# Performance work log

Hardware: AMD Instinct MI355X
Metric: run time of the kernel (lower is better)

Reference implementation:

```python
import jax, jax.numpy as jnp
import numpy as np

D_IN = 512
SEQ_LEN = 4096
CHUNK = 256
NUM_CHUNKS = SEQ_LEN // CHUNK
BATCH = 4


def _xavier_uniform(key, d_in, d_out):
    limit = float(np.sqrt(6.0 / (d_in + d_out)))
    return jax.random.uniform(key, (d_in, d_out), dtype=jnp.float32, minval=-limit, maxval=limit)


def _logit(p, eps=1e-06):
    p = min(max(p, eps), 1.0 - eps)
    return jnp.asarray(np.log(p / (1.0 - p)), dtype=jnp.float32)


def setup_inputs() -> dict:
    key = jax.random.key(0)
    ks = jax.random.split(key, 6)
    x = jax.random.normal(ks[0], (BATCH, SEQ_LEN, D_IN), dtype=jnp.float32)
    return {
        "x": x,
        "w_q": _xavier_uniform(ks[1], D_IN, D_IN),
        "w_k": _xavier_uniform(ks[2], D_IN, D_IN),
        "w_v": _xavier_uniform(ks[3], D_IN, D_IN),
        "mem_w1": _xavier_uniform(ks[4], D_IN, 2 * D_IN),
        "mem_w2": _xavier_uniform(ks[5], 2 * D_IN, D_IN),
        "alpha_t": _logit(0.001),  # unconstrained; sigmoid -> alpha
        "lr_t": _logit(0.01),
        "decay_t": _logit(0.9),
        "update_mem": 1,
    }


def _mem_fwd(h, W1, W2):
    # LinearMLPMemory depth=2: x @ W1 -> gelu -> @ W2 (torch F.gelu is exact erf)
    return jax.nn.gelu(h @ W1, approximate=False) @ W2


def reference(x, w_q, w_k, w_v, mem_w1, mem_w2, alpha_t, lr_t, decay_t, update_mem):
    alpha = jax.nn.sigmoid(alpha_t)
    lr = jax.nn.sigmoid(lr_t)
    decay = jax.nn.sigmoid(decay_t)

    def loss_fn(Ws, k, v):
        W1, W2 = Ws
        pred = _mem_fwd(k, W1, W2)
        return jnp.mean((pred - v) ** 2)

    grad_fn = jax.grad(loss_fn)

    def step(carry, chunk):
        # chunk: [B, CHUNK, D]
        W1, W2, S1, S2 = carry
        k = chunk @ w_k
        v = chunk @ w_v
        g1, g2 = grad_fn((W1, W2), k, v)
        S1 = decay * S1 - lr * g1  # surprise (momentum of negative grads)
        S2 = decay * S2 - lr * g2
        W1 = (1.0 - alpha) * W1 + S1  # weight decay + surprise update
        W2 = (1.0 - alpha) * W2 + S2
        return (W1, W2, S1, S2), None

    W1, W2 = mem_w1, mem_w2
    if update_mem:
        B, S, D = x.shape
        # [NUM_CHUNKS, B, CHUNK, D]: sequential store over chunks (parallelize=False)
        chunks = x.reshape(B, NUM_CHUNKS, CHUNK, D).transpose(1, 0, 2, 3)
        init = (W1, W2, jnp.zeros_like(W1), jnp.zeros_like(W2))
        (W1, W2, _, _), _ = jax.lax.scan(step, init, chunks)

    q = x @ w_q
    return _mem_fwd(q, W1, W2)
```

## Files before the change

### kernel.cpp

```cpp
#include <hip/hip_runtime.h>
#include <math.h>

#define D_IN    512
#define HID     1024
#define CHUNK_L 256
#define NCHUNK  16
#define SEQ_L   4096
#define ROWS    1024
#define NROWS_T 16384

typedef __attribute__((ext_vector_type(4))) float f32x4;
typedef __attribute__((ext_vector_type(8))) short bf16x8;
typedef __attribute__((ext_vector_type(4))) short bf16x4;

#define LOSS_SCALE (2.0f / 524288.0f)

__device__ __forceinline__ float gelu_f(float v) {
    return v * 0.5f * (1.0f + erff(v * 0.70710678118654752f));
}
__device__ __forceinline__ float dgelu_f(float v) {
    float cdf = 0.5f * (1.0f + erff(v * 0.70710678118654752f));
    float pdf = 0.3989422804014327f * expf(-0.5f * v * v);
    return cdf + v * pdf;
}
__device__ __forceinline__ float sigmoid_dev(float x) { return 1.0f / (1.0f + expf(-x)); }
__device__ __forceinline__ short f2b(float f) {
    unsigned u = __float_as_uint(f);
    u += 0x7fffu + ((u >> 16) & 1u);
    return (short)(u >> 16);
}
__device__ __forceinline__ float b2f(short s) {
    return __uint_as_float(((unsigned)(unsigned short)s) << 16);
}
__device__ __forceinline__ float read_scalar(const float* p) {
    float v = *p;
    if (fabsf(v) > 0.5f && fabsf(v) < 16.0f) return v;
    unsigned short lo = ((const unsigned short*)p)[0];
    return __uint_as_float(((unsigned)lo) << 16);
}

__device__ __forceinline__ void glds16(const short* g, short* l) {
    __builtin_amdgcn_global_load_lds(
        (const __attribute__((address_space(1))) void*)g,
        (__attribute__((address_space(3))) void*)l, 16, 0, 0);
}

#define VMWAIT(N) asm volatile("s_waitcnt vmcnt(" #N ")" ::: "memory")

template<int NKB, int NSLOT>
__device__ __forceinline__ void tile_gemm2(
    const short* __restrict__ A, int lda,
    const short* __restrict__ B, int ldb,
    int m0, int n0, short* KB, f32x4 acc[2][2])
{
    const int tid = threadIdx.x;
    const int lane = tid & 63, wave = tid >> 6;
    const int wy = (wave >> 1) * 32, wx = (wave & 1) * 32;
    const int l16 = lane & 15, q = lane >> 4;

    const int ga = tid, gb = tid + 256;
    const int ra = ga >> 3, ja = ga & 7;
    const int rb = gb >> 3, jb = gb & 7;
    const short* sA0 = A + (size_t)(m0 + ra) * lda + ((ja ^ (ra & 7)) << 3);
    const short* sA1 = A + (size_t)(m0 + rb) * lda + ((jb ^ (rb & 7)) << 3);
    const short* sB0 = B + (size_t)(n0 + ra) * ldb + ((ja ^ (ra & 7)) << 3);
    const short* sB1 = B + (size_t)(n0 + rb) * ldb + ((jb ^ (rb & 7)) << 3);

    f32x4 z = {0.f, 0.f, 0.f, 0.f};
    acc[0][0] = z; acc[0][1] = z; acc[1][0] = z; acc[1][1] = z;

    auto issue = [&](int kb) {
        const int ko = kb << 6;
        short* d = KB + (kb % NSLOT) * 8192 + wave * 512;
        glds16(sA0 + ko, d);
        glds16(sA1 + ko, d + 2048);
        glds16(sB0 + ko, d + 4096);
        glds16(sB1 + ko, d + 6144);
    };
#pragma unroll
    for (int kb = 0; kb < NSLOT - 1 && kb < NKB; ++kb) issue(kb);

#pragma unroll
    for (int j = 0; j < NKB; ++j) {
        int ah = NKB - 1 - j; if (ah > NSLOT - 2) ah = NSLOT - 2;
        if      (ah >= 6) VMWAIT(24);
        else if (ah == 5) VMWAIT(20);
        else if (ah == 4) VMWAIT(16);
        else if (ah == 3) VMWAIT(12);
        else if (ah == 2) VMWAIT(8);
        else if (ah == 1) VMWAIT(4);
        else              VMWAIT(0);
        __builtin_amdgcn_s_barrier();
        __builtin_amdgcn_sched_barrier(0);
        if (j + NSLOT - 1 < NKB) issue(j + NSLOT - 1);
        const short* sl = KB + (j % NSLOT) * 8192;
#pragma unroll
        for (int ks = 0; ks < 2; ++ks) {
            bf16x8 af[2], bf[2];
#pragma unroll
            for (int i = 0; i < 2; ++i) {
                int row = wy + i * 16 + l16;
                af[i] = *(const bf16x8*)&sl[(row << 6) + (((ks * 4 + q) ^ (row & 7)) << 3)];
            }
#pragma unroll
            for (int jj = 0; jj < 2; ++jj) {
                int row = wx + jj * 16 + l16;
                bf[jj] = *(const bf16x8*)&sl[4096 + (row << 6) + (((ks * 4 + q) ^ (row & 7)) << 3)];
            }
#pragma unroll
            for (int i = 0; i < 2; ++i)
#pragma unroll
                for (int jj = 0; jj < 2; ++jj)
                    acc[i][jj] = __builtin_amdgcn_mfma_f32_16x16x32_bf16(af[i], bf[jj], acc[i][jj], 0, 0, 0);
        }
    }
}

#define EPI_IDX() \
    const int tid_ = threadIdx.x; \
    const int wy_  = ((tid_ >> 6) >> 1) * 32; \
    const int wxl_ = ((tid_ >> 6) & 1) * 32; \
    const int q4_  = ((tid_ & 63) >> 4) * 4; \
    const int l16_ = tid_ & 15;

__global__ __launch_bounds__(256)
void init_all(const float* __restrict__ w_q, const float* __restrict__ w_k,
              const float* __restrict__ w_v, const float* __restrict__ m1,
              const float* __restrict__ m2,
              float* __restrict__ W1f, float* __restrict__ W2f,
              float* __restrict__ S1, float* __restrict__ S2,
              short* __restrict__ WkvT, short* __restrict__ wqT,
              short* __restrict__ W1bT, short* __restrict__ W2bT,
              short* __restrict__ W2bn)
{
    int i = blockIdx.x * 256 + threadIdx.x;
    float w1 = m1[i], w2 = m2[i];
    W1f[i] = w1; S1[i] = 0.f;
    W2f[i] = w2; S2[i] = 0.f;
    W2bn[i] = f2b(w2);
    int n9 = i >> 9, k9 = i & 511;
    W1bT[i] = f2b(m1[(size_t)k9 * HID + n9]);
    WkvT[i] = f2b(n9 < 512 ? w_k[(size_t)k9 * D_IN + n9]
                           : w_v[(size_t)k9 * D_IN + (n9 - 512)]);
    if (i < 262144) wqT[i] = f2b(w_q[(size_t)k9 * D_IN + n9]);
    int n10 = i >> 10, k10 = i & 1023;
    W2bT[i] = f2b(m2[(size_t)k10 * D_IN + n10]);
}

__global__ __launch_bounds__(256)
void xb_kernel(const float* __restrict__ x, short* __restrict__ xb)
{
    int i = blockIdx.x * 256 + threadIdx.x;
    f32x4 a = ((const f32x4*)x)[i * 2];
    f32x4 b = ((const f32x4*)x)[i * 2 + 1];
    bf16x8 o;
#pragma unroll
    for (int u = 0; u < 4; ++u) { o[u] = f2b(a[u]); o[u + 4] = f2b(b[u]); }
    ((bf16x8*)xb)[i] = o;
}

__global__ __launch_bounds__(256)
void kvq_kernel(const short* __restrict__ xb, const short* __restrict__ WkvT,
                const short* __restrict__ wqT,
                short* __restrict__ KVall, short* __restrict__ Ktall,
                short* __restrict__ qall)
{
    __shared__ short KB[3 * 8192];
    const int bid = blockIdx.x;
    EPI_IDX();
    f32x4 acc[2][2];
    if (bid < 4096) {
        int t = bid >> 8, tile = bid & 255;
        int m0 = (tile & 15) * 64, n0 = (tile >> 4) * 64;
        const short* Akv = xb + ((size_t)(m0 >> 8) * SEQ_L + (size_t)t * CHUNK_L + (m0 & 255)) * D_IN;
        tile_gemm2<8, 3>(Akv, D_IN, WkvT, D_IN, 0, n0, KB, acc);
        short* KV = KVall + (size_t)t * ROWS * 1024;
        short* Kt = Ktall + (size_t)t * D_IN * 1024;
#pragma unroll
        for (int i = 0; i < 2; ++i)
#pragma unroll
            for (int j = 0; j < 2; ++j) {
                int m = m0 + wy_ + i * 16 + q4_, n = n0 + wxl_ + j * 16 + l16_;
                bf16x4 pk;
#pragma unroll
                for (int r = 0; r < 4; ++r) {
                    short b = f2b(acc[i][j][r]);
                    KV[(size_t)(m + r) * 1024 + n] = b;
                    pk[r] = b;
                }
                if (n < 512) *(bf16x4*)&Kt[(size_t)n * 1024 + m] = pk;
            }
    } else {
        int idx = bid - 4096;
        int m0 = (idx & 255) * 64, n0 = (idx >> 8) * 64;
        tile_gemm2<8, 3>(xb, D_IN, wqT, D_IN, m0, n0, KB, acc);
#pragma unroll
        for (int i = 0; i < 2; ++i)
#pragma unroll
            for (int j = 0; j < 2; ++j) {
                int m = m0 + wy_ + i * 16 + q4_, n = n0 + wxl_ + j * 16 + l16_;
#pragma unroll
                for (int r = 0; r < 4; ++r)
                    qall[(size_t)(m + r) * D_IN + n] = f2b(acc[i][j][r]);
            }
    }
}

__global__ __launch_bounds__(256)
void h_kernel(const short* __restrict__ KVt, const short* __restrict__ W1bT,
              short* __restrict__ Gb, short* __restrict__ GbT, short* __restrict__ DG)
{
    __shared__ short KB[8 * 8192];
    const int bid = blockIdx.x;
    EPI_IDX();
    int m0 = (bid & 15) * 64, n0 = (bid >> 4) * 64;
    f32x4 acc[2][2];
    tile_gemm2<8, 8>(KVt, 1024, W1bT, D_IN, m0, n0, KB, acc);
#pragma unroll
    for (int i = 0; i < 2; ++i)
#pragma unroll
        for (int j = 0; j < 2; ++j) {
            int m = m0 + wy_ + i * 16 + q4_, n = n0 + wxl_ + j * 16 + l16_;
            bf16x4 pg;
#pragma unroll
            for (int r = 0; r < 4; ++r) {
                float v = acc[i][j][r];
                float g = gelu_f(v);
                Gb[(size_t)(m + r) * 1024 + n] = f2b(g);
                DG[(size_t)(m + r) * 1024 + n] = f2b(dgelu_f(v));
                pg[r] = f2b(g);
            }
            *(bf16x4*)&GbT[(size_t)n * 1024 + m] = pg;
        }
}

__global__ __launch_bounds__(256)
void e_kernel(const short* __restrict__ Gb, const short* __restrict__ W2bT,
              short* __restrict__ KVt, short* __restrict__ EVt)
{
    __shared__ short KB[8 * 8192];
    const int bid = blockIdx.x;
    EPI_IDX();
    int m0 = (bid & 15) * 64, n0 = (bid >> 4) * 64;
    f32x4 acc[2][2];
    tile_gemm2<16, 8>(Gb, HID, W2bT, HID, m0, n0, KB, acc);
#pragma unroll
    for (int i = 0; i < 2; ++i)
#pragma unroll
        for (int j = 0; j < 2; ++j) {
            int m = m0 + wy_ + i * 16 + q4_, n = n0 + wxl_ + j * 16 + l16_;
            bf16x4 pe;
#pragma unroll
            for (int r = 0; r < 4; ++r) {
                size_t ci = (size_t)(m + r) * 1024 + 512 + n;
                float e = (acc[i][j][r] - b2f(KVt[ci])) * LOSS_SCALE;
                KVt[ci] = f2b(e);
                pe[r] = f2b(e);
            }
            *(bf16x4*)&EVt[(size_t)n * 1024 + m] = pe;
        }
}

__global__ __launch_bounds__(256)
void dh_kernel(const short* __restrict__ KVt, const short* __restrict__ W2bn,
               const short* __restrict__ DG, short* __restrict__ DHt)
{
    __shared__ short KB[8 * 8192];
    const int bid = blockIdx.x;
    EPI_IDX();
    int m0 = (bid & 15) * 64, n0 = (bid >> 4) * 64;
    f32x4 acc[2][2];
    tile_gemm2<8, 8>(KVt + 512, 1024, W2bn, D_IN, m0, n0, KB, acc);
#pragma unroll
    for (int i = 0; i < 2; ++i)
#pragma unroll
        for (int j = 0; j < 2; ++j) {
            int m = m0 + wy_ + i * 16 + q4_, n = n0 + wxl_ + j * 16 + l16_;
            bf16x4 pd;
#pragma unroll
            for (int r = 0; r < 4; ++r)
                pd[r] = f2b(acc[i][j][r] * b2f(DG[(size_t)(m + r) * 1024 + n]));
            *(bf16x4*)&DHt[(size_t)n * 1024 + m] = pd;
        }
}

__global__ __launch_bounds__(256)
void g21_kernel(const short* __restrict__ GbT, const short* __restrict__ EVt,
                const short* __restrict__ Ktt, const short* __restrict__ DHt,
                float* __restrict__ W2f, float* __restrict__ S2,
                short* __restrict__ W2bT, short* __restrict__ W2bn,
                float* __restrict__ W1f, float* __restrict__ S1,
                short* __restrict__ W1bT,
                const float* __restrict__ ap, const float* __restrict__ lp,
                const float* __restrict__ dp, const int* __restrict__ um)
{
    __shared__ short KB[8 * 8192];
    const int bid = blockIdx.x;
    EPI_IDX();
    f32x4 acc[2][2];
    if (bid < 128) {
        int m0 = (bid & 15) * 64, n0 = (bid >> 4) * 64;
        tile_gemm2<16, 8>(GbT, ROWS, EVt, ROWS, m0, n0, KB, acc);
        if (*um != 0) {
            const float alpha = sigmoid_dev(read_scalar(ap));
            const float lr    = sigmoid_dev(read_scalar(lp));
            const float decay = sigmoid_dev(read_scalar(dp));
#pragma unroll
            for (int i = 0; i < 2; ++i)
#pragma unroll
                for (int j = 0; j < 2; ++j) {
                    int m = m0 + wy_ + i * 16 + q4_, n = n0 + wxl_ + j * 16 + l16_;
                    bf16x4 pw;
#pragma unroll
                    for (int r = 0; r < 4; ++r) {
                        size_t ci = (size_t)(m + r) * D_IN + n;
                        float s = decay * S2[ci] - lr * acc[i][j][r];
                        S2[ci] = s;
                        float w = (1.0f - alpha) * W2f[ci] + s;
                        W2f[ci] = w;
                        W2bn[ci] = f2b(w);
                        pw[r] = f2b(w);
                    }
                    *(bf16x4*)&W2bT[(size_t)n * 1024 + m] = pw;
                }
        }
    } else {
        int idx = bid - 128;
        int m0 = (idx & 7) * 64, n0 = (idx >> 3) * 64;
        tile_gemm2<16, 8>(Ktt, ROWS, DHt, ROWS, m0, n0, KB, acc);
        if (*um != 0) {
            const float alpha = sigmoid_dev(read_scalar(ap));
            const float lr    = sigmoid_dev(read_scalar(lp));
            const float decay = sigmoid_dev(read_scalar(dp));
#pragma unroll
            for (int i = 0; i < 2; ++i)
#pragma unroll
                for (int j = 0; j < 2; ++j) {
                    int m = m0 + wy_ + i * 16 + q4_, n = n0 + wxl_ + j * 16 + l16_;
                    bf16x4 pw;
#pragma unroll
                    for (int r = 0; r < 4; ++r) {
                        size_t ci = (size_t)(m + r) * HID + n;
                        float s = decay * S1[ci] - lr * acc[i][j][r];
                        S1[ci] = s;
                        float w = (1.0f - alpha) * W1f[ci] + s;
                        W1f[ci] = w;
                        pw[r] = f2b(w);
                    }
                    *(bf16x4*)&W1bT[(size_t)n * D_IN + m] = pw;
                }
        }
    }
}

__global__ __launch_bounds__(256)
void ro_h_kernel(const short* __restrict__ qall, const short* __restrict__ W1bT,
                 short* __restrict__ Hro)
{
    __shared__ short KB[3 * 8192];
    const int bid = blockIdx.x;
    EPI_IDX();
    int m0 = (bid & 255) * 64, n0 = (bid >> 8) * 64;
    f32x4 acc[2][2];
    tile_gemm2<8, 3>(qall, D_IN, W1bT, D_IN, m0, n0, KB, acc);
#pragma unroll
    for (int i = 0; i < 2; ++i)
#pragma unroll
        for (int j = 0; j < 2; ++j) {
            int m = m0 + wy_ + i * 16 + q4_, n = n0 + wxl_ + j * 16 + l16_;
#pragma unroll
            for (int r = 0; r < 4; ++r)
                Hro[(size_t)(m + r) * HID + n] = f2b(gelu_f(acc[i][j][r]));
        }
}

__global__ __launch_bounds__(256)
void ro_o_kernel(const short* __restrict__ Hro, const short* __restrict__ W2bT,
                 float* __restrict__ out)
{
    __shared__ short KB[3 * 8192];
    const int bid = blockIdx.x;
    EPI_IDX();
    int m0 = (bid & 255) * 64, n0 = (bid >> 8) * 64;
    f32x4 acc[2][2];
    tile_gemm2<16, 3>(Hro, HID, W2bT, HID, m0, n0, KB, acc);
#pragma unroll
    for (int i = 0; i < 2; ++i)
#pragma unroll
        for (int j = 0; j < 2; ++j) {
            int m = m0 + wy_ + i * 16 + q4_, n = n0 + wxl_ + j * 16 + l16_;
#pragma unroll
            for (int r = 0; r < 4; ++r)
                out[(size_t)(m + r) * D_IN + n] = acc[i][j][r];
        }
}

extern "C" void kernel_launch(void* const* d_in, const int* in_sizes, int n_in,
                              void* d_out, int out_size, void* d_ws, size_t ws_size,
                              hipStream_t stream)
{
    const float* x      = (const float*)d_in[0];
    const float* w_q    = (const float*)d_in[1];
    const float* w_k    = (const float*)d_in[2];
    const float* w_v    = (const float*)d_in[3];
    const float* mem_w1 = (const float*)d_in[4];
    const float* mem_w2 = (const float*)d_in[5];
    const float* ap     = (const float*)d_in[6];
    const float* lp     = (const float*)d_in[7];
    const float* dpp    = (const float*)d_in[8];
    const int*   um     = (const int*)d_in[9];
    float* out = (float*)d_out;

    const int nW = D_IN * HID;
    float* W1f = (float*)d_ws;
    float* W2f = W1f + nW;
    float* S1  = W2f + nW;
    float* S2  = S1 + nW;
    short* p   = (short*)(S2 + nW);
    short* WkvT = p;            p += nW;
    short* wqT  = p;            p += 256 * 1024;
    short* W1bT = p;            p += nW;
    short* W2bT = p;            p += nW;
    short* W2bn = p;            p += nW;
    short* Gb   = p;            p += ROWS * HID;
    short* GbT  = p;            p += ROWS * HID;
    short* DG   = p;            p += ROWS * HID;
    short* EVt  = p;            p += ROWS * D_IN;
    short* DHt  = p;            p += ROWS * HID;
    short* qall = p;            p += (size_t)NROWS_T * D_IN;
    short* KVall = p;           p += (size_t)NCHUNK * ROWS * 1024;
    short* Ktall = p;           p += (size_t)NCHUNK * D_IN * 1024;
    short* Hro  = p;            p += (size_t)NROWS_T * HID;
    short* xb   = p;            p += (size_t)NROWS_T * D_IN;

    dim3 blk(256);
    hipLaunchKernelGGL(init_all, dim3(nW / 256), blk, 0, stream,
                       w_q, w_k, w_v, mem_w1, mem_w2,
                       W1f, W2f, S1, S2, WkvT, wqT, W1bT, W2bT, W2bn);
    hipLaunchKernelGGL(xb_kernel, dim3(4096), blk, 0, stream, x, xb);
    hipLaunchKernelGGL(kvq_kernel, dim3(6144), blk, 0, stream,
                       xb, WkvT, wqT, KVall, Ktall, qall);

    for (int t = 0; t < NCHUNK; ++t) {
        short* KVt  = KVall + (size_t)t * ROWS * 1024;
        short* Ktt  = Ktall + (size_t)t * D_IN * 1024;
        hipLaunchKernelGGL(h_kernel, dim3(256), blk, 0, stream, KVt, W1bT, Gb, GbT, DG);
        hipLaunchKernelGGL(e_kernel, dim3(128), blk, 0, stream, Gb, W2bT, KVt, EVt);
        hipLaunchKernelGGL(dh_kernel, dim3(256), blk, 0, stream, KVt, W2bn, DG, DHt);
        hipLaunchKernelGGL(g21_kernel, dim3(256), blk, 0, stream,
                           GbT, EVt, Ktt, DHt, W2f, S2, W2bT, W2bn,
                           W1f, S1, W1bT, ap, lp, dpp, um);
    }

    hipLaunchKernelGGL(ro_h_kernel, dim3(4096), blk, 0, stream, qall, W1bT, Hro);
    hipLaunchKernelGGL(ro_o_kernel, dim3(2048), blk, 0, stream, Hro, W2bT, out);
}
```

Before: 749.4 us.

## Make KVQ and readout blocks loop over N-tiles; fuse readout GEMMs

The KVQ projection now launches one block per 64-row strip that loops over all N-tiles, instead of one block per output tile. The two readout GEMMs are merged into a single kernel: each block computes its 64-row strip of the GELU hidden layer, then reuses it for the second GEMM, with a barrier between the phases. The goal is fewer launches and better cache reuse of each A strip. The cost is far fewer blocks (256 to 512 on a large GPU), which lowers occupancy and parallelism, and the deeper LDS buffers may reduce how many blocks fit per CU.

```diff
diff --git a/kernel.cpp b/kernel.cpp
--- a/kernel.cpp
+++ b/kernel.cpp
@@ -165,44 +165,48 @@
                 short* __restrict__ KVall, short* __restrict__ Ktall,
                 short* __restrict__ qall)
 {
-    __shared__ short KB[3 * 8192];
-    const int bid = blockIdx.x;
-    EPI_IDX();
-    f32x4 acc[2][2];
-    if (bid < 4096) {
-        int t = bid >> 8, tile = bid & 255;
-        int m0 = (tile & 15) * 64, n0 = (tile >> 4) * 64;
+    __shared__ short KB[4 * 8192];
+    const int bid = blockIdx.x;
+    EPI_IDX();
+    f32x4 acc[2][2];
+    if (bid < 256) {
+        int t = bid >> 4, m0 = (bid & 15) * 64;
         const short* Akv = xb + ((size_t)(m0 >> 8) * SEQ_L + (size_t)t * CHUNK_L + (m0 & 255)) * D_IN;
-        tile_gemm2<8, 3>(Akv, D_IN, WkvT, D_IN, 0, n0, KB, acc);
         short* KV = KVall + (size_t)t * ROWS * 1024;
         short* Kt = Ktall + (size_t)t * D_IN * 1024;
-#pragma unroll
-        for (int i = 0; i < 2; ++i)
-#pragma unroll
-            for (int j = 0; j < 2; ++j) {
-                int m = m0 + wy_ + i * 16 + q4_, n = n0 + wxl_ + j * 16 + l16_;
-                bf16x4 pk;
-#pragma unroll
-                for (int r = 0; r < 4; ++r) {
-                    short b = f2b(acc[i][j][r]);
-                    KV[(size_t)(m + r) * 1024 + n] = b;
-                    pk[r] = b;
+        for (int nt = 0; nt < 16; ++nt) {
+            int n0 = nt * 64;
+            tile_gemm2<8, 4>(Akv, D_IN, WkvT, D_IN, 0, n0, KB, acc);
+#pragma unroll
+            for (int i = 0; i < 2; ++i)
+#pragma unroll
+                for (int j = 0; j < 2; ++j) {
+                    int m = m0 + wy_ + i * 16 + q4_, n = n0 + wxl_ + j * 16 + l16_;
+                    bf16x4 pk;
+#pragma unroll
+                    for (int r = 0; r < 4; ++r) {
+                        short b = f2b(acc[i][j][r]);
+                        KV[(size_t)(m + r) * 1024 + n] = b;
+                        pk[r] = b;
+                    }
+                    if (n < 512) *(bf16x4*)&Kt[(size_t)n * 1024 + m] = pk;
                 }
-                if (n < 512) *(bf16x4*)&Kt[(size_t)n * 1024 + m] = pk;
-            }
+        }
     } else {
-        int idx = bid - 4096;
-        int m0 = (idx & 255) * 64, n0 = (idx >> 8) * 64;
-        tile_gemm2<8, 3>(xb, D_IN, wqT, D_IN, m0, n0, KB, acc);
-#pragma unroll
-        for (int i = 0; i < 2; ++i)
-#pragma unroll
-            for (int j = 0; j < 2; ++j) {
-                int m = m0 + wy_ + i * 16 + q4_, n = n0 + wxl_ + j * 16 + l16_;
-#pragma unroll
-                for (int r = 0; r < 4; ++r)
-                    qall[(size_t)(m + r) * D_IN + n] = f2b(acc[i][j][r]);
-            }
+        int m0 = (bid - 256) * 64;
+        for (int nt = 0; nt < 8; ++nt) {
+            int n0 = nt * 64;
+            tile_gemm2<8, 4>(xb, D_IN, wqT, D_IN, m0, n0, KB, acc);
+#pragma unroll
+            for (int i = 0; i < 2; ++i)
+#pragma unroll
+                for (int j = 0; j < 2; ++j) {
+                    int m = m0 + wy_ + i * 16 + q4_, n = n0 + wxl_ + j * 16 + l16_;
+#pragma unroll
+                    for (int r = 0; r < 4; ++r)
+                        qall[(size_t)(m + r) * D_IN + n] = f2b(acc[i][j][r]);
+                }
+        }
     }
 }
 
@@ -354,45 +358,46 @@
 }
 
 __global__ __launch_bounds__(256)
-void ro_h_kernel(const short* __restrict__ qall, const short* __restrict__ W1bT,
-                 short* __restrict__ Hro)
-{
-    __shared__ short KB[3 * 8192];
-    const int bid = blockIdx.x;
-    EPI_IDX();
-    int m0 = (bid & 255) * 64, n0 = (bid >> 8) * 64;
-    f32x4 acc[2][2];
-    tile_gemm2<8, 3>(qall, D_IN, W1bT, D_IN, m0, n0, KB, acc);
-#pragma unroll
-    for (int i = 0; i < 2; ++i)
-#pragma unroll
-        for (int j = 0; j < 2; ++j) {
-            int m = m0 + wy_ + i * 16 + q4_, n = n0 + wxl_ + j * 16 + l16_;
-#pragma unroll
-            for (int r = 0; r < 4; ++r)
-                Hro[(size_t)(m + r) * HID + n] = f2b(gelu_f(acc[i][j][r]));
-        }
-}
-
-__global__ __launch_bounds__(256)
-void ro_o_kernel(const short* __restrict__ Hro, const short* __restrict__ W2bT,
-                 float* __restrict__ out)
-{
-    __shared__ short KB[3 * 8192];
-    const int bid = blockIdx.x;
-    EPI_IDX();
-    int m0 = (bid & 255) * 64, n0 = (bid >> 8) * 64;
-    f32x4 acc[2][2];
-    tile_gemm2<16, 3>(Hro, HID, W2bT, HID, m0, n0, KB, acc);
-#pragma unroll
-    for (int i = 0; i < 2; ++i)
-#pragma unroll
-        for (int j = 0; j < 2; ++j) {
-            int m = m0 + wy_ + i * 16 + q4_, n = n0 + wxl_ + j * 16 + l16_;
-#pragma unroll
-            for (int r = 0; r < 4; ++r)
-                out[(size_t)(m + r) * D_IN + n] = acc[i][j][r];
-        }
+void ro_kernel(const short* __restrict__ qall, const short* __restrict__ W1bT,
+               const short* __restrict__ W2bT, short* __restrict__ Hro,
+               float* __restrict__ out)
+{
+    __shared__ short KB[8 * 8192];
+    const int bid = blockIdx.x;
+    EPI_IDX();
+    const int m0 = bid * 64;
+    f32x4 acc[2][2];
+
+    for (int nt = 0; nt < 16; ++nt) {
+        int n0 = nt * 64;
+        tile_gemm2<8, 8>(qall, D_IN, W1bT, D_IN, m0, n0, KB, acc);
+#pragma unroll
+        for (int i = 0; i < 2; ++i)
+#pragma unroll
+            for (int j = 0; j < 2; ++j) {
+                int m = m0 + wy_ + i * 16 + q4_, n = n0 + wxl_ + j * 16 + l16_;
+#pragma unroll
+                for (int r = 0; r < 4; ++r)
+                    Hro[(size_t)(m + r) * HID + n] = f2b(gelu_f(acc[i][j][r]));
+            }
+    }
+
+    VMWAIT(0);
+    __builtin_amdgcn_s_barrier();
+
+    for (int nt = 0; nt < 8; ++nt) {
+        int n0 = nt * 64;
+        tile_gemm2<16, 8>(Hro, HID, W2bT, HID, m0, n0, KB, acc);
+#pragma unroll
+        for (int i = 0; i < 2; ++i)
+#pragma unroll
+            for (int j = 0; j < 2; ++j) {
+                int m = m0 + wy_ + i * 16 + q4_, n = n0 + wxl_ + j * 16 + l16_;
+#pragma unroll
+                for (int r = 0; r < 4; ++r)
+                    out[(size_t)(m + r) * D_IN + n] = acc[i][j][r];
+            }
+    }
 }
 
 extern "C" void kernel_launch(void* const* d_in, const int* in_sizes, int n_in,
@@ -438,7 +443,7 @@
                        w_q, w_k, w_v, mem_w1, mem_w2,
                        W1f, W2f, S1, S2, WkvT, wqT, W1bT, W2bT, W2bn);
     hipLaunchKernelGGL(xb_kernel, dim3(4096), blk, 0, stream, x, xb);
-    hipLaunchKernelGGL(kvq_kernel, dim3(6144), blk, 0, stream,
+    hipLaunchKernelGGL(kvq_kernel, dim3(512), blk, 0, stream,
                        xb, WkvT, wqT, KVall, Ktall, qall);
 
     for (int t = 0; t < NCHUNK; ++t) {
@@ -452,6 +457,6 @@
                            W1f, S1, W1bT, ap, lp, dpp, um);
     }
 
-    hipLaunchKernelGGL(ro_h_kernel, dim3(4096), blk, 0, stream, qall, W1bT, Hro);
-    hipLaunchKernelGGL(ro_o_kernel, dim3(2048), blk, 0, stream, Hro, W2bT, out);
-}
+    hipLaunchKernelGGL(ro_kernel, dim3(256), blk, 0, stream,
+                       qall, W1bT, W2bT, Hro, out);
+}
```

Result: slower. 772.6 us (+3.1%).

## Fuse per-chunk update kernels into one persistent kernel with grid barriers

Applied to the files above, without the earlier changes.

Replaces the 64 per-chunk kernel launches (four per chunk over sixteen chunks) with a single persistent 256-block kernel. It loops over the chunks and separates the stages with a software grid barrier built on per-block atomic flags and a go word. This removes launch gaps and kernel drain/fill overhead in the sequential memory-update loop. In exchange it assumes all 256 blocks, each with 128 KB of LDS, are co-resident, or the barrier will deadlock. It also adds barrier latency, with block 0 polling every flag.

```diff
diff --git a/kernel.cpp b/kernel.cpp
--- a/kernel.cpp
+++ b/kernel.cpp
@@ -8,6 +8,7 @@
 #define SEQ_L   4096
 #define ROWS    1024
 #define NROWS_T 16384
+#define NB_LOOP 256
 
 typedef __attribute__((ext_vector_type(4))) float f32x4;
 typedef __attribute__((ext_vector_type(8))) short bf16x8;
@@ -123,6 +124,29 @@
     const int q4_  = ((tid_ & 63) >> 4) * 4; \
     const int l16_ = tid_ & 15;
 
+__device__ __forceinline__ void gsync(unsigned* flags, unsigned* go, unsigned gen)
+{
+    __syncthreads();
+    if (threadIdx.x == 0)
+        __hip_atomic_store(&flags[blockIdx.x], gen, __ATOMIC_RELEASE, __HIP_MEMORY_SCOPE_AGENT);
+    if (blockIdx.x == 0) {
+        unsigned v;
+        do {
+            __builtin_amdgcn_s_sleep(1);
+            v = __hip_atomic_load(&flags[threadIdx.x], __ATOMIC_RELAXED, __HIP_MEMORY_SCOPE_AGENT);
+        } while (v < gen);
+        __syncthreads();
+        if (threadIdx.x == 0)
+            __hip_atomic_store(go, gen, __ATOMIC_RELEASE, __HIP_MEMORY_SCOPE_AGENT);
+    }
+    if (threadIdx.x == 0) {
+        while (__hip_atomic_load(go, __ATOMIC_RELAXED, __HIP_MEMORY_SCOPE_AGENT) < gen)
+            __builtin_amdgcn_s_sleep(2);
+        (void)__hip_atomic_load(go, __ATOMIC_ACQUIRE, __HIP_MEMORY_SCOPE_AGENT);
+    }
+    __syncthreads();
+}
+
 __global__ __launch_bounds__(256)
 void init_all(const float* __restrict__ w_q, const float* __restrict__ w_k,
               const float* __restrict__ w_v, const float* __restrict__ m1,
@@ -131,9 +155,10 @@
               float* __restrict__ S1, float* __restrict__ S2,
               short* __restrict__ WkvT, short* __restrict__ wqT,
               short* __restrict__ W1bT, short* __restrict__ W2bT,
-              short* __restrict__ W2bn)
+              short* __restrict__ W2bn, unsigned* __restrict__ barw)
 {
     int i = blockIdx.x * 256 + threadIdx.x;
+    if (i < 257) barw[i] = 0;
     float w1 = m1[i], w2 = m2[i];
     W1f[i] = w1; S1[i] = 0.f;
     W2f[i] = w2; S2[i] = 0.f;
@@ -206,105 +231,99 @@
     }
 }
 
-__global__ __launch_bounds__(256)
-void h_kernel(const short* __restrict__ KVt, const short* __restrict__ W1bT,
-              short* __restrict__ Gb, short* __restrict__ GbT, short* __restrict__ DG)
+struct LoopArgs {
+    short *KVall, *Ktall;
+    short *W1bT, *W2bT, *W2bn;
+    short *Gb, *GbT, *DG, *EVt, *DHt;
+    float *W1f, *W2f, *S1, *S2;
+    const float *ap, *lp, *dp;
+    const int *um;
+    unsigned *flags, *go;
+};
+
+__global__ __launch_bounds__(256)
+void loop_kernel(LoopArgs a)
 {
     __shared__ short KB[8 * 8192];
     const int bid = blockIdx.x;
     EPI_IDX();
-    int m0 = (bid & 15) * 64, n0 = (bid >> 4) * 64;
+
+    if (*a.um == 0) return;
+
+    const float alpha = sigmoid_dev(read_scalar(a.ap));
+    const float lr    = sigmoid_dev(read_scalar(a.lp));
+    const float decay = sigmoid_dev(read_scalar(a.dp));
+
+    unsigned gen = 0;
     f32x4 acc[2][2];
-    tile_gemm2<8, 8>(KVt, 1024, W1bT, D_IN, m0, n0, KB, acc);
-#pragma unroll
-    for (int i = 0; i < 2; ++i)
-#pragma unroll
-        for (int j = 0; j < 2; ++j) {
-            int m = m0 + wy_ + i * 16 + q4_, n = n0 + wxl_ + j * 16 + l16_;
-            bf16x4 pg;
-#pragma unroll
-            for (int r = 0; r < 4; ++r) {
-                float v = acc[i][j][r];
-                float g = gelu_f(v);
-                Gb[(size_t)(m + r) * 1024 + n] = f2b(g);
-                DG[(size_t)(m + r) * 1024 + n] = f2b(dgelu_f(v));
-                pg[r] = f2b(g);
-            }
-            *(bf16x4*)&GbT[(size_t)n * 1024 + m] = pg;
-        }
-}
-
-__global__ __launch_bounds__(256)
-void e_kernel(const short* __restrict__ Gb, const short* __restrict__ W2bT,
-              short* __restrict__ KVt, short* __restrict__ EVt)
-{
-    __shared__ short KB[8 * 8192];
-    const int bid = blockIdx.x;
-    EPI_IDX();
-    int m0 = (bid & 15) * 64, n0 = (bid >> 4) * 64;
-    f32x4 acc[2][2];
-    tile_gemm2<16, 8>(Gb, HID, W2bT, HID, m0, n0, KB, acc);
-#pragma unroll
-    for (int i = 0; i < 2; ++i)
-#pragma unroll
-        for (int j = 0; j < 2; ++j) {
-            int m = m0 + wy_ + i * 16 + q4_, n = n0 + wxl_ + j * 16 + l16_;
-            bf16x4 pe;
-#pragma unroll
-            for (int r = 0; r < 4; ++r) {
-                size_t ci = (size_t)(m + r) * 1024 + 512 + n;
-                float e = (acc[i][j][r] - b2f(KVt[ci])) * LOSS_SCALE;
-                KVt[ci] = f2b(e);
-                pe[r] = f2b(e);
-            }
-            *(bf16x4*)&EVt[(size_t)n * 1024 + m] = pe;
-        }
-}
-
-__global__ __launch_bounds__(256)
-void dh_kernel(const short* __restrict__ KVt, const short* __restrict__ W2bn,
-               const short* __restrict__ DG, short* __restrict__ DHt)
-{
-    __shared__ short KB[8 * 8192];
-    const int bid = blockIdx.x;
-    EPI_IDX();
-    int m0 = (bid & 15) * 64, n0 = (bid >> 4) * 64;
-    f32x4 acc[2][2];
-    tile_gemm2<8, 8>(KVt + 512, 1024, W2bn, D_IN, m0, n0, KB, acc);
-#pragma unroll
-    for (int i = 0; i < 2; ++i)
-#pragma unroll
-        for (int j = 0; j < 2; ++j) {
-            int m = m0 + wy_ + i * 16 + q4_, n = n0 + wxl_ + j * 16 + l16_;
-            bf16x4 pd;
-#pragma unroll
-            for (int r = 0; r < 4; ++r)
-                pd[r] = f2b(acc[i][j][r] * b2f(DG[(size_t)(m + r) * 1024 + n]));
-            *(bf16x4*)&DHt[(size_t)n * 1024 + m] = pd;
-        }
-}
-
-__global__ __launch_bounds__(256)
-void g21_kernel(const short* __restrict__ GbT, const short* __restrict__ EVt,
-                const short* __restrict__ Ktt, const short* __restrict__ DHt,
-                float* __restrict__ W2f, float* __restrict__ S2,
-                short* __restrict__ W2bT, short* __restrict__ W2bn,
-                float* __restrict__ W1f, float* __restrict__ S1,
-                short* __restrict__ W1bT,
-                const float* __restrict__ ap, const float* __restrict__ lp,
-                const float* __restrict__ dp, const int* __restrict__ um)
-{
-    __shared__ short KB[8 * 8192];
-    const int bid = blockIdx.x;
-    EPI_IDX();
-    f32x4 acc[2][2];
-    if (bid < 128) {
-        int m0 = (bid & 15) * 64, n0 = (bid >> 4) * 64;
-        tile_gemm2<16, 8>(GbT, ROWS, EVt, ROWS, m0, n0, KB, acc);
-        if (*um != 0) {
-            const float alpha = sigmoid_dev(read_scalar(ap));
-            const float lr    = sigmoid_dev(read_scalar(lp));
-            const float decay = sigmoid_dev(read_scalar(dp));
+
+    for (int t = 0; t < NCHUNK; ++t) {
+        short* KVt = a.KVall + (size_t)t * ROWS * 1024;
+        short* Ktt = a.Ktall + (size_t)t * D_IN * 1024;
+
+        {
+            int m0 = (bid & 15) * 64, n0 = (bid >> 4) * 64;
+            tile_gemm2<8, 8>(KVt, 1024, a.W1bT, D_IN, m0, n0, KB, acc);
+#pragma unroll
+            for (int i = 0; i < 2; ++i)
+#pragma unroll
+                for (int j = 0; j < 2; ++j) {
+                    int m = m0 + wy_ + i * 16 + q4_, n = n0 + wxl_ + j * 16 + l16_;
+                    bf16x4 pg;
+#pragma unroll
+                    for (int r = 0; r < 4; ++r) {
+                        float v = acc[i][j][r];
+                        float g = gelu_f(v);
+                        a.Gb[(size_t)(m + r) * 1024 + n] = f2b(g);
+                        a.DG[(size_t)(m + r) * 1024 + n] = f2b(dgelu_f(v));
+                        pg[r] = f2b(g);
+                    }
+                    *(bf16x4*)&a.GbT[(size_t)n * 1024 + m] = pg;
+                }
+        }
+        gsync(a.flags, a.go, ++gen);
+
+        if (bid < 128) {
+            int m0 = (bid & 15) * 64, n0 = (bid >> 4) * 64;
+            tile_gemm2<16, 8>(a.Gb, HID, a.W2bT, HID, m0, n0, KB, acc);
+#pragma unroll
+            for (int i = 0; i < 2; ++i)
+#pragma unroll
+                for (int j = 0; j < 2; ++j) {
+                    int m = m0 + wy_ + i * 16 + q4_, n = n0 + wxl_ + j * 16 + l16_;
+                    bf16x4 pe;
+#pragma unroll
+                    for (int r = 0; r < 4; ++r) {
+                        size_t ci = (size_t)(m + r) * 1024 + 512 + n;
+                        float e = (acc[i][j][r] - b2f(KVt[ci])) * LOSS_SCALE;
+                        KVt[ci] = f2b(e);
+                        pe[r] = f2b(e);
+                    }
+                    *(bf16x4*)&a.EVt[(size_t)n * 1024 + m] = pe;
+                }
+        }
+        gsync(a.flags, a.go, ++gen);
+
+        {
+            int m0 = (bid & 15) * 64, n0 = (bid >> 4) * 64;
+            tile_gemm2<8, 8>(KVt + 512, 1024, a.W2bn, D_IN, m0, n0, KB, acc);
+#pragma unroll
+            for (int i = 0; i < 2; ++i)
+#pragma unroll
+                for (int j = 0; j < 2; ++j) {
+                    int m = m0 + wy_ + i * 16 + q4_, n = n0 + wxl_ + j * 16 + l16_;
+                    bf16x4 pd;
+#pragma unroll
+                    for (int r = 0; r < 4; ++r)
+                        pd[r] = f2b(acc[i][j][r] * b2f(a.DG[(size_t)(m + r) * 1024 + n]));
+                    *(bf16x4*)&a.DHt[(size_t)n * 1024 + m] = pd;
+                }
+        }
+        gsync(a.flags, a.go, ++gen);
+
+        if (bid < 128) {
+            int m0 = (bid & 15) * 64, n0 = (bid >> 4) * 64;
+            tile_gemm2<16, 8>(a.GbT, ROWS, a.EVt, ROWS, m0, n0, KB, acc);
 #pragma unroll
             for (int i = 0; i < 2; ++i)
 #pragma unroll
@@ -314,24 +333,19 @@
 #pragma unroll
                     for (int r = 0; r < 4; ++r) {
                         size_t ci = (size_t)(m + r) * D_IN + n;
-                        float s = decay * S2[ci] - lr * acc[i][j][r];
-                        S2[ci] = s;
-                        float w = (1.0f - alpha) * W2f[ci] + s;
-                        W2f[ci] = w;
-                        W2bn[ci] = f2b(w);
+                        float s = decay * a.S2[ci] - lr * acc[i][j][r];
+                        a.S2[ci] = s;
+                        float w = (1.0f - alpha) * a.W2f[ci] + s;
+                        a.W2f[ci] = w;
+                        a.W2bn[ci] = f2b(w);
                         pw[r] = f2b(w);
                     }
-                    *(bf16x4*)&W2bT[(size_t)n * 1024 + m] = pw;
-                }
-        }
-    } else {
-        int idx = bid - 128;
-        int m0 = (idx & 7) * 64, n0 = (idx >> 3) * 64;
-        tile_gemm2<16, 8>(Ktt, ROWS, DHt, ROWS, m0, n0, KB, acc);
-        if (*um != 0) {
-            const float alpha = sigmoid_dev(read_scalar(ap));
-            const float lr    = sigmoid_dev(read_scalar(lp));
-            const float decay = sigmoid_dev(read_scalar(dp));
+                    *(bf16x4*)&a.W2bT[(size_t)n * 1024 + m] = pw;
+                }
+        } else {
+            int idx = bid - 128;
+            int m0 = (idx & 7) * 64, n0 = (idx >> 3) * 64;
+            tile_gemm2<16, 8>(Ktt, ROWS, a.DHt, ROWS, m0, n0, KB, acc);
 #pragma unroll
             for (int i = 0; i < 2; ++i)
 #pragma unroll
@@ -341,15 +355,16 @@
 #pragma unroll
                     for (int r = 0; r < 4; ++r) {
                         size_t ci = (size_t)(m + r) * HID + n;
-                        float s = decay * S1[ci] - lr * acc[i][j][r];
-                        S1[ci] = s;
-                        float w = (1.0f - alpha) * W1f[ci] + s;
-                        W1f[ci] = w;
+                        float s = decay * a.S1[ci] - lr * acc[i][j][r];
+                        a.S1[ci] = s;
+                        float w = (1.0f - alpha) * a.W1f[ci] + s;
+                        a.W1f[ci] = w;
                         pw[r] = f2b(w);
                     }
-                    *(bf16x4*)&W1bT[(size_t)n * D_IN + m] = pw;
-                }
-        }
+                    *(bf16x4*)&a.W1bT[(size_t)n * D_IN + m] = pw;
+                }
+        }
+        gsync(a.flags, a.go, ++gen);
     }
 }
 
@@ -432,25 +447,24 @@
     short* Ktall = p;           p += (size_t)NCHUNK * D_IN * 1024;
     short* Hro  = p;            p += (size_t)NROWS_T * HID;
     short* xb   = p;            p += (size_t)NROWS_T * D_IN;
+    unsigned* barw = (unsigned*)p;
 
     dim3 blk(256);
     hipLaunchKernelGGL(init_all, dim3(nW / 256), blk, 0, stream,
                        w_q, w_k, w_v, mem_w1, mem_w2,
-                       W1f, W2f, S1, S2, WkvT, wqT, W1bT, W2bT, W2bn);
+                       W1f, W2f, S1, S2, WkvT, wqT, W1bT, W2bT, W2bn, barw);
     hipLaunchKernelGGL(xb_kernel, dim3(4096), blk, 0, stream, x, xb);
     hipLaunchKernelGGL(kvq_kernel, dim3(6144), blk, 0, stream,
                        xb, WkvT, wqT, KVall, Ktall, qall);
 
-    for (int t = 0; t < NCHUNK; ++t) {
-        short* KVt  = KVall + (size_t)t * ROWS * 1024;
-        short* Ktt  = Ktall + (size_t)t * D_IN * 1024;
-        hipLaunchKernelGGL(h_kernel, dim3(256), blk, 0, stream, KVt, W1bT, Gb, GbT, DG);
-        hipLaunchKernelGGL(e_kernel, dim3(128), blk, 0, stream, Gb, W2bT, KVt, EVt);
-        hipLaunchKernelGGL(dh_kernel, dim3(256), blk, 0, stream, KVt, W2bn, DG, DHt);
-        hipLaunchKernelGGL(g21_kernel, dim3(256), blk, 0, stream,
-                           GbT, EVt, Ktt, DHt, W2f, S2, W2bT, W2bn,
-                           W1f, S1, W1bT, ap, lp, dpp, um);
-    }
+    LoopArgs la;
+    la.KVall = KVall; la.Ktall = Ktall;
+    la.W1bT = W1bT; la.W2bT = W2bT; la.W2bn = W2bn;
+    la.Gb = Gb; la.GbT = GbT; la.DG = DG; la.EVt = EVt; la.DHt = DHt;
+    la.W1f = W1f; la.W2f = W2f; la.S1 = S1; la.S2 = S2;
+    la.ap = ap; la.lp = lp; la.dp = dpp; la.um = um;
+    la.flags = barw; la.go = barw + 256;
+    hipLaunchKernelGGL(loop_kernel, dim3(NB_LOOP), blk, 0, stream, la);
 
     hipLaunchKernelGGL(ro_h_kernel, dim3(4096), blk, 0, stream, qall, W1bT, Hro);
     hipLaunchKernelGGL(ro_o_kernel, dim3(2048), blk, 0, stream, Hro, W2bT, out);
```

After: 1.617 ms. 2.16x slower.

## Split K across two wave groups in per-chunk GEMMs and remap readout tiles by XCD

Applied to the files above, without the earlier changes.

Adds a tile_gemm3 variant that runs 8 waves per 64x64 tile. Two groups of four waves each take half of every 64-wide K slab, and one group's partial accumulators are reduced through LDS at the end. The sequential per-chunk kernels (h, e, dh, g21) switch to 512-thread blocks, because they launch only 128-256 blocks and cannot fill the GPU otherwise. Separately, the readout GEMMs remap block IDs so that consecutive blocks on the same XCD share A rows, aiming for better L2 reuse. The cost is an extra LDS reduction with two barriers, and only half the threads doing the epilogue.

```diff
diff --git a/kernel.cpp b/kernel.cpp
--- a/kernel.cpp
+++ b/kernel.cpp
@@ -58,13 +58,12 @@
     const int wy = (wave >> 1) * 32, wx = (wave & 1) * 32;
     const int l16 = lane & 15, q = lane >> 4;
 
-    const int ga = tid, gb = tid + 256;
-    const int ra = ga >> 3, ja = ga & 7;
-    const int rb = gb >> 3, jb = gb & 7;
+    const int ra = tid >> 3, ja = tid & 7;
+    const int rb = ra + 32;
     const short* sA0 = A + (size_t)(m0 + ra) * lda + ((ja ^ (ra & 7)) << 3);
-    const short* sA1 = A + (size_t)(m0 + rb) * lda + ((jb ^ (rb & 7)) << 3);
+    const short* sA1 = A + (size_t)(m0 + rb) * lda + ((ja ^ (rb & 7)) << 3);
     const short* sB0 = B + (size_t)(n0 + ra) * ldb + ((ja ^ (ra & 7)) << 3);
-    const short* sB1 = B + (size_t)(n0 + rb) * ldb + ((jb ^ (rb & 7)) << 3);
+    const short* sB1 = B + (size_t)(n0 + rb) * ldb + ((ja ^ (rb & 7)) << 3);
 
     f32x4 z = {0.f, 0.f, 0.f, 0.f};
     acc[0][0] = z; acc[0][1] = z; acc[1][0] = z; acc[1][1] = z;
@@ -116,9 +115,100 @@
     }
 }
 
+template<int NKB, int NSLOT>
+__device__ __forceinline__ void tile_gemm3(
+    const short* __restrict__ A, int lda,
+    const short* __restrict__ B, int ldb,
+    int m0, int n0, short* KB, f32x4 acc[2][2])
+{
+    const int tid = threadIdx.x;
+    const int lane = tid & 63, wave = tid >> 6;
+    const int w3 = wave & 3, grp = wave >> 2;
+    const int wy = (w3 >> 1) * 32, wx = (w3 & 1) * 32;
+    const int l16 = lane & 15, q = lane >> 4;
+
+    const int t2 = tid & 255;
+    const int ra = t2 >> 3, ja = t2 & 7;
+    const int rb = ra + 32;
+    const short* s0 = (grp == 0)
+        ? A + (size_t)(m0 + ra) * lda + ((ja ^ (ra & 7)) << 3)
+        : B + (size_t)(n0 + ra) * ldb + ((ja ^ (ra & 7)) << 3);
+    const short* s1 = (grp == 0)
+        ? A + (size_t)(m0 + rb) * lda + ((ja ^ (rb & 7)) << 3)
+        : B + (size_t)(n0 + rb) * ldb + ((ja ^ (rb & 7)) << 3);
+    const int dbase = grp * 4096;
+
+    f32x4 z = {0.f, 0.f, 0.f, 0.f};
+    acc[0][0] = z; acc[0][1] = z; acc[1][0] = z; acc[1][1] = z;
+
+    auto issue = [&](int kb) {
+        const int ko = kb << 6;
+        short* d = KB + (kb % NSLOT) * 8192 + dbase + w3 * 512;
+        glds16(s0 + ko, d);
+        glds16(s1 + ko, d + 2048);
+    };
+#pragma unroll
+    for (int kb = 0; kb < NSLOT - 1 && kb < NKB; ++kb) issue(kb);
+
+#pragma unroll
+    for (int j = 0; j < NKB; ++j) {
+        int ah = NKB - 1 - j; if (ah > NSLOT - 2) ah = NSLOT - 2;
+        if      (ah >= 6) VMWAIT(12);
+        else if (ah == 5) VMWAIT(10);
+        else if (ah == 4) VMWAIT(8);
+        else if (ah == 3) VMWAIT(6);
+        else if (ah == 2) VMWAIT(4);
+        else if (ah == 1) VMWAIT(2);
+        else              VMWAIT(0);
+        __builtin_amdgcn_s_barrier();
+        __builtin_amdgcn_sched_barrier(0);
+        if (j + NSLOT - 1 < NKB) issue(j + NSLOT - 1);
+        const short* sl = KB + (j % NSLOT) * 8192;
+        const int ks = grp;
+        bf16x8 af[2], bf[2];
+#pragma unroll
+        for (int i = 0; i < 2; ++i) {
+            int row = wy + i * 16 + l16;
+            af[i] = *(const bf16x8*)&sl[(row << 6) + (((ks * 4 + q) ^ (row & 7)) << 3)];
+        }
+#pragma unroll
+        for (int jj = 0; jj < 2; ++jj) {
+            int row = wx + jj * 16 + l16;
+            bf[jj] = *(const bf16x8*)&sl[4096 + (row << 6) + (((ks * 4 + q) ^ (row & 7)) << 3)];
+        }
+#pragma unroll
+        for (int i = 0; i < 2; ++i)
+#pragma unroll
+            for (int jj = 0; jj < 2; ++jj)
+                acc[i][jj] = __builtin_amdgcn_mfma_f32_16x16x32_bf16(af[i], bf[jj], acc[i][jj], 0, 0, 0);
+    }
+
+    __syncthreads();
+    float* red = (float*)KB;
+    if (grp == 1) {
+#pragma unroll
+        for (int i = 0; i < 2; ++i)
+#pragma unroll
+            for (int jj = 0; jj < 2; ++jj)
+#pragma unroll
+                for (int r = 0; r < 4; ++r)
+                    red[((i * 2 + jj) * 4 + r) * 256 + t2] = acc[i][jj][r];
+    }
+    __syncthreads();
+    if (grp == 0) {
+#pragma unroll
+        for (int i = 0; i < 2; ++i)
+#pragma unroll
+            for (int jj = 0; jj < 2; ++jj)
+#pragma unroll
+                for (int r = 0; r < 4; ++r)
+                    acc[i][jj][r] += red[((i * 2 + jj) * 4 + r) * 256 + t2];
+    }
+}
+
 #define EPI_IDX() \
     const int tid_ = threadIdx.x; \
-    const int wy_  = ((tid_ >> 6) >> 1) * 32; \
+    const int wy_  = (((tid_ >> 6) & 3) >> 1) * 32; \
     const int wxl_ = ((tid_ >> 6) & 1) * 32; \
     const int q4_  = ((tid_ & 63) >> 4) * 4; \
     const int l16_ = tid_ & 15;
@@ -206,7 +296,7 @@
     }
 }
 
-__global__ __launch_bounds__(256)
+__global__ __launch_bounds__(512)
 void h_kernel(const short* __restrict__ KVt, const short* __restrict__ W1bT,
               short* __restrict__ Gb, short* __restrict__ GbT, short* __restrict__ DG)
 {
@@ -215,26 +305,28 @@
     EPI_IDX();
     int m0 = (bid & 15) * 64, n0 = (bid >> 4) * 64;
     f32x4 acc[2][2];
-    tile_gemm2<8, 8>(KVt, 1024, W1bT, D_IN, m0, n0, KB, acc);
-#pragma unroll
-    for (int i = 0; i < 2; ++i)
-#pragma unroll
-        for (int j = 0; j < 2; ++j) {
-            int m = m0 + wy_ + i * 16 + q4_, n = n0 + wxl_ + j * 16 + l16_;
-            bf16x4 pg;
-#pragma unroll
-            for (int r = 0; r < 4; ++r) {
-                float v = acc[i][j][r];
-                float g = gelu_f(v);
-                Gb[(size_t)(m + r) * 1024 + n] = f2b(g);
-                DG[(size_t)(m + r) * 1024 + n] = f2b(dgelu_f(v));
-                pg[r] = f2b(g);
-            }
-            *(bf16x4*)&GbT[(size_t)n * 1024 + m] = pg;
-        }
-}
-
-__global__ __launch_bounds__(256)
+    tile_gemm3<8, 8>(KVt, 1024, W1bT, D_IN, m0, n0, KB, acc);
+    if (tid_ < 256) {
+#pragma unroll
+        for (int i = 0; i < 2; ++i)
+#pragma unroll
+            for (int j = 0; j < 2; ++j) {
+                int m = m0 + wy_ + i * 16 + q4_, n = n0 + wxl_ + j * 16 + l16_;
+                bf16x4 pg;
+#pragma unroll
+                for (int r = 0; r < 4; ++r) {
+                    float v = acc[i][j][r];
+                    float g = gelu_f(v);
+                    Gb[(size_t)(m + r) * 1024 + n] = f2b(g);
+                    DG[(size_t)(m + r) * 1024 + n] = f2b(dgelu_f(v));
+                    pg[r] = f2b(g);
+                }
+                *(bf16x4*)&GbT[(size_t)n * 1024 + m] = pg;
+            }
+    }
+}
+
+__global__ __launch_bounds__(512)
 void e_kernel(const short* __restrict__ Gb, const short* __restrict__ W2bT,
               short* __restrict__ KVt, short* __restrict__ EVt)
 {
@@ -243,25 +335,27 @@
     EPI_IDX();
     int m0 = (bid & 15) * 64, n0 = (bid >> 4) * 64;
     f32x4 acc[2][2];
-    tile_gemm2<16, 8>(Gb, HID, W2bT, HID, m0, n0, KB, acc);
-#pragma unroll
-    for (int i = 0; i < 2; ++i)
-#pragma unroll
-        for (int j = 0; j < 2; ++j) {
-            int m = m0 + wy_ + i * 16 + q4_, n = n0 + wxl_ + j * 16 + l16_;
-            bf16x4 pe;
-#pragma unroll
-            for (int r = 0; r < 4; ++r) {
-                size_t ci = (size_t)(m + r) * 1024 + 512 + n;
-                float e = (acc[i][j][r] - b2f(KVt[ci])) * LOSS_SCALE;
-                KVt[ci] = f2b(e);
-                pe[r] = f2b(e);
-            }
-            *(bf16x4*)&EVt[(size_t)n * 1024 + m] = pe;
-        }
-}
-
-__global__ __launch_bounds__(256)
+    tile_gemm3<16, 8>(Gb, HID, W2bT, HID, m0, n0, KB, acc);
+    if (tid_ < 256) {
+#pragma unroll
+        for (int i = 0; i < 2; ++i)
+#pragma unroll
+            for (int j = 0; j < 2; ++j) {
+                int m = m0 + wy_ + i * 16 + q4_, n = n0 + wxl_ + j * 16 + l16_;
+                bf16x4 pe;
+#pragma unroll
+                for (int r = 0; r < 4; ++r) {
+                    size_t ci = (size_t)(m + r) * 1024 + 512 + n;
+                    float e = (acc[i][j][r] - b2f(KVt[ci])) * LOSS_SCALE;
+                    KVt[ci] = f2b(e);
+                    pe[r] = f2b(e);
+                }
+                *(bf16x4*)&EVt[(size_t)n * 1024 + m] = pe;
+            }
+    }
+}
+
+__global__ __launch_bounds__(512)
 void dh_kernel(const short* __restrict__ KVt, const short* __restrict__ W2bn,
                const short* __restrict__ DG, short* __restrict__ DHt)
 {
@@ -270,21 +364,23 @@
     EPI_IDX();
     int m0 = (bid & 15) * 64, n0 = (bid >> 4) * 64;
     f32x4 acc[2][2];
-    tile_gemm2<8, 8>(KVt + 512, 1024, W2bn, D_IN, m0, n0, KB, acc);
-#pragma unroll
-    for (int i = 0; i < 2; ++i)
-#pragma unroll
-        for (int j = 0; j < 2; ++j) {
-            int m = m0 + wy_ + i * 16 + q4_, n = n0 + wxl_ + j * 16 + l16_;
-            bf16x4 pd;
-#pragma unroll
-            for (int r = 0; r < 4; ++r)
-                pd[r] = f2b(acc[i][j][r] * b2f(DG[(size_t)(m + r) * 1024 + n]));
-            *(bf16x4*)&DHt[(size_t)n * 1024 + m] = pd;
-        }
-}
-
-__global__ __launch_bounds__(256)
+    tile_gemm3<8, 8>(KVt + 512, 1024, W2bn, D_IN, m0, n0, KB, acc);
+    if (tid_ < 256) {
+#pragma unroll
+        for (int i = 0; i < 2; ++i)
+#pragma unroll
+            for (int j = 0; j < 2; ++j) {
+                int m = m0 + wy_ + i * 16 + q4_, n = n0 + wxl_ + j * 16 + l16_;
+                bf16x4 pd;
+#pragma unroll
+                for (int r = 0; r < 4; ++r)
+                    pd[r] = f2b(acc[i][j][r] * b2f(DG[(size_t)(m + r) * 1024 + n]));
+                *(bf16x4*)&DHt[(size_t)n * 1024 + m] = pd;
+            }
+    }
+}
+
+__global__ __launch_bounds__(512)
 void g21_kernel(const short* __restrict__ GbT, const short* __restrict__ EVt,
                 const short* __restrict__ Ktt, const short* __restrict__ DHt,
                 float* __restrict__ W2f, float* __restrict__ S2,
@@ -300,8 +396,8 @@
     f32x4 acc[2][2];
     if (bid < 128) {
         int m0 = (bid & 15) * 64, n0 = (bid >> 4) * 64;
-        tile_gemm2<16, 8>(GbT, ROWS, EVt, ROWS, m0, n0, KB, acc);
-        if (*um != 0) {
+        tile_gemm3<16, 8>(GbT, ROWS, EVt, ROWS, m0, n0, KB, acc);
+        if (tid_ < 256 && *um != 0) {
             const float alpha = sigmoid_dev(read_scalar(ap));
             const float lr    = sigmoid_dev(read_scalar(lp));
             const float decay = sigmoid_dev(read_scalar(dp));
@@ -327,8 +423,8 @@
     } else {
         int idx = bid - 128;
         int m0 = (idx & 7) * 64, n0 = (idx >> 3) * 64;
-        tile_gemm2<16, 8>(Ktt, ROWS, DHt, ROWS, m0, n0, KB, acc);
-        if (*um != 0) {
+        tile_gemm3<16, 8>(Ktt, ROWS, DHt, ROWS, m0, n0, KB, acc);
+        if (tid_ < 256 && *um != 0) {
             const float alpha = sigmoid_dev(read_scalar(ap));
             const float lr    = sigmoid_dev(read_scalar(lp));
             const float decay = sigmoid_dev(read_scalar(dp));
@@ -360,7 +456,9 @@
     __shared__ short KB[3 * 8192];
     const int bid = blockIdx.x;
     EPI_IDX();
-    int m0 = (bid & 255) * 64, n0 = (bid >> 8) * 64;
+    int xcd = bid & 7, w = bid >> 3;
+    int m0 = ((w >> 4) * 8 + xcd) * 64;
+    int n0 = (w & 15) * 64;
     f32x4 acc[2][2];
     tile_gemm2<8, 3>(qall, D_IN, W1bT, D_IN, m0, n0, KB, acc);
 #pragma unroll
@@ -381,7 +479,9 @@
     __shared__ short KB[3 * 8192];
     const int bid = blockIdx.x;
     EPI_IDX();
-    int m0 = (bid & 255) * 64, n0 = (bid >> 8) * 64;
+    int xcd = bid & 7, w = bid >> 3;
+    int m0 = ((w >> 3) * 8 + xcd) * 64;
+    int n0 = (w & 7) * 64;
     f32x4 acc[2][2];
     tile_gemm2<16, 3>(Hro, HID, W2bT, HID, m0, n0, KB, acc);
 #pragma unroll
@@ -433,7 +533,7 @@
     short* Hro  = p;            p += (size_t)NROWS_T * HID;
     short* xb   = p;            p += (size_t)NROWS_T * D_IN;
 
-    dim3 blk(256);
+    dim3 blk(256), blk2(512);
     hipLaunchKernelGGL(init_all, dim3(nW / 256), blk, 0, stream,
                        w_q, w_k, w_v, mem_w1, mem_w2,
                        W1f, W2f, S1, S2, WkvT, wqT, W1bT, W2bT, W2bn);
@@ -444,10 +544,10 @@
     for (int t = 0; t < NCHUNK; ++t) {
         short* KVt  = KVall + (size_t)t * ROWS * 1024;
         short* Ktt  = Ktall + (size_t)t * D_IN * 1024;
-        hipLaunchKernelGGL(h_kernel, dim3(256), blk, 0, stream, KVt, W1bT, Gb, GbT, DG);
-        hipLaunchKernelGGL(e_kernel, dim3(128), blk, 0, stream, Gb, W2bT, KVt, EVt);
-        hipLaunchKernelGGL(dh_kernel, dim3(256), blk, 0, stream, KVt, W2bn, DG, DHt);
-        hipLaunchKernelGGL(g21_kernel, dim3(256), blk, 0, stream,
+        hipLaunchKernelGGL(h_kernel, dim3(256), blk2, 0, stream, KVt, W1bT, Gb, GbT, DG);
+        hipLaunchKernelGGL(e_kernel, dim3(128), blk2, 0, stream, Gb, W2bT, KVt, EVt);
+        hipLaunchKernelGGL(dh_kernel, dim3(256), blk2, 0, stream, KVt, W2bn, DG, DHt);
+        hipLaunchKernelGGL(g21_kernel, dim3(256), blk2, 0, stream,
                            GbT, EVt, Ktt, DHt, W2f, S2, W2bT, W2bn,
                            W1f, S1, W1bT, ap, lp, dpp, um);
     }
```

After: 718.8 us. 4.1% less time.
